# Kernel tuning notes

Measured on AMD Instinct MI355X. Metric: run time of the kernel, lower is better.

The kernel has to match this reference:

```python
import jax, jax.numpy as jnp
import numpy as np

TEMPERATURE = 0.5

def setup_inputs() -> dict:
    key = jax.random.key(0)
    ks = jax.random.split(key, 8)
    B, D, H, T, C = 4096, 1024, 4096, 8, 1000
    return {
        "x": jax.random.normal(ks[0], (B, D), jnp.float32),
        "signatures": jax.random.normal(ks[1], (T, D), jnp.float32) * 0.1,
        "W_up": jax.random.normal(ks[2], (T, H, D), jnp.float32) * (1.0 / np.sqrt(D)),
        "b_up": jax.random.normal(ks[3], (T, H), jnp.float32) * 0.01,
        "W_down": jax.random.normal(ks[4], (T, D, H), jnp.float32) * (1.0 / np.sqrt(H)),
        "b_down": jax.random.normal(ks[5], (T, D), jnp.float32) * 0.01,
        "W_cls": jax.random.normal(ks[6], (C, D), jnp.float32) * (1.0 / np.sqrt(D)),
        "b_cls": jax.random.normal(ks[7], (C,), jnp.float32) * 0.01,
    }

def reference(x, signatures, W_up, b_up, W_down, b_down, W_cls, b_cls):
    # Soft routing: scores (B, T), softmax weights at temperature 0.5
    scores = x @ signatures.T
    indices = jnp.argmax(scores, axis=-1)
    weights = jax.nn.softmax(scores / TEMPERATURE, axis=-1)
    # Batched per-tile FFN: Linear -> GELU(exact) -> Linear, all tiles at once
    h = jax.nn.gelu(jnp.einsum('bd,thd->bth', x, W_up) + b_up[None], approximate=False)  # (B,T,H)
    tile_out = jnp.einsum('bth,tdh->btd', h, W_down) + b_down[None]                      # (B,T,D)
    # Weighted combine + residual
    outputs = jnp.einsum('bt,btd->bd', weights, tile_out) + x
    logits = outputs @ W_cls.T + b_cls
    return logits, indices, weights
```

## Files before the change

### kernel.cpp

```cpp
#include <hip/hip_runtime.h>
#include <stdint.h>


typedef __attribute__((ext_vector_type(8))) __bf16 bf16x8;
typedef __attribute__((ext_vector_type(4))) float f32x4;

__device__ __forceinline__ unsigned short f2bf(float f) {
  union { float f; unsigned int u; } c; c.f = f;
  unsigned int u = c.u;
  u += 0x7FFFu + ((u >> 16) & 1u);
  return (unsigned short)(u >> 16);
}

__device__ __forceinline__ float gelu_fast(float x) {
  float x2 = x * x;
  float p = __builtin_fmaf(0.044715f * x2, x, x);
  float e = __expf(-1.5957691216057308f * p);
  return x / (1.0f + e);
}

__device__ __forceinline__ void gload16(const void* g, void* l) {
  __builtin_amdgcn_global_load_lds((const __attribute__((address_space(1))) void*)g,
                                   (__attribute__((address_space(3))) void*)l,
                                   16, 0, 0);
}

__global__ void conv_bf16(const float* __restrict__ in, unsigned short* __restrict__ out, int n4) {
  int i = blockIdx.x * blockDim.x + threadIdx.x;
  if (i >= n4) return;
  float4 v = reinterpret_cast<const float4*>(in)[i];
  ushort4 o;
  o.x = f2bf(v.x); o.y = f2bf(v.y); o.z = f2bf(v.z); o.w = f2bf(v.w);
  reinterpret_cast<ushort4*>(out)[i] = o;
}

__global__ void conv_wdn(const float* __restrict__ in, unsigned short* __restrict__ out) {
  int i = blockIdx.x * blockDim.x + threadIdx.x;
  int idx = i * 4;
  int h = idx & 4095;
  int d = (idx >> 12) & 1023;
  int t = idx >> 22;
  float4 v = *reinterpret_cast<const float4*>(in + (size_t)(t * 1024 + d) * 4096 + h);
  ushort4 o;
  o.x = f2bf(v.x); o.y = f2bf(v.y); o.z = f2bf(v.z); o.w = f2bf(v.w);
  *reinterpret_cast<ushort4*>(out + (size_t)d * 32768 + t * 4096 + h) = o;
}

__global__ void conv_wcls(const float* __restrict__ in, unsigned short* __restrict__ out) {
  int i = blockIdx.x * blockDim.x + threadIdx.x;
  int idx = i * 4;
  int row = idx >> 10;
  float4 v = make_float4(0.f, 0.f, 0.f, 0.f);
  if (row < 1000) v = *reinterpret_cast<const float4*>(in + row * 1024 + (idx & 1023));
  ushort4 o;
  o.x = f2bf(v.x); o.y = f2bf(v.y); o.z = f2bf(v.z); o.w = f2bf(v.w);
  reinterpret_cast<ushort4*>(out)[i] = o;
}

__global__ void score_init(const float* __restrict__ x, const float* __restrict__ sig,
                           const float* __restrict__ b_down,
                           float* __restrict__ w_ws, float* __restrict__ out_init,
                           float* __restrict__ w_out, float* __restrict__ idx_out) {
  const int b = blockIdx.x;
  const int tid = threadIdx.x;
  const int lane = tid & 63;
  const int wave = tid >> 6;
  const float* xr = x + (size_t)b * 1024;

  float p[8];
  #pragma unroll
  for (int t = 0; t < 8; ++t) p[t] = 0.f;

  for (int k = tid; k < 1024; k += 256) {
    float xv = xr[k];
    #pragma unroll
    for (int t = 0; t < 8; ++t) p[t] += xv * sig[t * 1024 + k];
  }
  #pragma unroll
  for (int t = 0; t < 8; ++t) {
    #pragma unroll
    for (int off = 32; off > 0; off >>= 1) p[t] += __shfl_down(p[t], off);
  }
  __shared__ float red[4][8];
  __shared__ float wsh[8];
  if (lane == 0) {
    #pragma unroll
    for (int t = 0; t < 8; ++t) red[wave][t] = p[t];
  }
  __syncthreads();
  if (tid == 0) {
    float s[8];
    #pragma unroll
    for (int t = 0; t < 8; ++t) s[t] = red[0][t] + red[1][t] + red[2][t] + red[3][t];
    int amax = 0; float mx = s[0];
    #pragma unroll
    for (int t = 1; t < 8; ++t) { if (s[t] > mx) { mx = s[t]; amax = t; } }
    float e[8], sum = 0.f;
    #pragma unroll
    for (int t = 0; t < 8; ++t) { e[t] = expf((s[t] - mx) * 2.0f); sum += e[t]; }
    float inv = 1.0f / sum;
    #pragma unroll
    for (int t = 0; t < 8; ++t) {
      float wv = e[t] * inv;
      wsh[t] = wv;
      w_out[(size_t)b * 8 + t] = wv;
      w_ws[(size_t)b * 8 + t] = wv;
    }
    idx_out[b] = (float)amax;
  }
  __syncthreads();
  for (int d = tid; d < 1024; d += 256) {
    float acc = xr[d];
    #pragma unroll
    for (int t = 0; t < 8; ++t) acc += wsh[t] * b_down[t * 1024 + d];
    out_init[(size_t)b * 1024 + d] = acc;
  }
}

template <int BN, int EPI>
__global__ __launch_bounds__(256, 2) void gemm_k(
    const unsigned short* __restrict__ A, int lda,
    const unsigned short* __restrict__ Bm, int ldb,
    int K,
    float* __restrict__ Cf, int ldc, int nvalid,
    unsigned short* __restrict__ Ch, int ldh,
    const float* __restrict__ bias,
    const float* __restrict__ wcol) {
  constexpr int FN = BN / 32;
  constexpr int AISS = 4;
  constexpr int BISS = BN / 32;

  __shared__ unsigned short As[128 * 64];
  __shared__ unsigned short Bs[BN * 64];

  if (EPI == 3) {
    size_t kz = (size_t)blockIdx.z * K;
    A += kz;
    Bm += kz;
    Cf += (size_t)blockIdx.z * 4194304;
  }

  const int tid  = threadIdx.x;
  const int lane = tid & 63;
  const int wave = tid >> 6;
  const int m0 = blockIdx.y * 128;
  const int n0 = blockIdx.x * BN;
  const int lr = lane & 15;
  const int lg = lane >> 4;
  const int wm = (wave >> 1) * 64;
  const int wn = (wave & 1) * (BN / 2);
  const int sw = (lr & 7) << 4;

  f32x4 acc[4][FN];
  #pragma unroll
  for (int i = 0; i < 4; ++i)
    #pragma unroll
    for (int j = 0; j < FN; ++j)
      #pragma unroll
      for (int q = 0; q < 4; ++q) acc[i][j][q] = 0.f;

  const char* Ab = (const char*)As;
  const char* Bb = (const char*)Bs;
  const int Lw = wave * 1024 + lane * 16;

  for (int k0 = 0; k0 < K; k0 += 64) {
    #pragma unroll
    for (int it = 0; it < AISS; ++it) {
      int L = it * 4096 + Lw;
      int row = L >> 7;
      int cb = (L & 127) ^ ((row & 7) << 4);
      const unsigned short* g = A + (size_t)(m0 + row) * lda + k0 + (cb >> 1);
      gload16(g, (void*)((char*)As + it * 4096 + wave * 1024));
    }
    #pragma unroll
    for (int it = 0; it < BISS; ++it) {
      int L = it * 4096 + Lw;
      int row = L >> 7;
      int cb = (L & 127) ^ ((row & 7) << 4);
      const unsigned short* g = Bm + (size_t)(n0 + row) * ldb + k0 + (cb >> 1);
      gload16(g, (void*)((char*)Bs + it * 4096 + wave * 1024));
    }
    asm volatile("s_waitcnt vmcnt(0)" ::: "memory");
    __syncthreads();

    #pragma unroll
    for (int kk = 0; kk < 2; ++kk) {
      bf16x8 a[4], bfr[FN];
      const int cbase = (kk << 6) + (lg << 4);
      #pragma unroll
      for (int mi = 0; mi < 4; ++mi) {
        int r = wm + mi * 16 + lr;
        a[mi] = *(const bf16x8*)(Ab + (r << 7) + (cbase ^ sw));
      }
      #pragma unroll
      for (int ni = 0; ni < FN; ++ni) {
        int r = wn + ni * 16 + lr;
        bfr[ni] = *(const bf16x8*)(Bb + (r << 7) + (cbase ^ sw));
      }
      #pragma unroll
      for (int mi = 0; mi < 4; ++mi)
        #pragma unroll
        for (int ni = 0; ni < FN; ++ni)
          acc[mi][ni] = __builtin_amdgcn_mfma_f32_16x16x32_bf16(a[mi], bfr[ni], acc[mi][ni], 0, 0, 0);
    }
    __syncthreads();
  }

  const int tblk = n0 >> 12;
  #pragma unroll
  for (int mi = 0; mi < 4; ++mi) {
    float wrow[4];
    if (EPI == 0) {
      #pragma unroll
      for (int r = 0; r < 4; ++r)
        wrow[r] = wcol[(size_t)(m0 + wm + mi * 16 + lg * 4 + r) * 8 + tblk];
    }
    #pragma unroll
    for (int ni = 0; ni < FN; ++ni) {
      int gn = n0 + wn + ni * 16 + lr;
      #pragma unroll
      for (int r = 0; r < 4; ++r) {
        int gm = m0 + wm + mi * 16 + lg * 4 + r;
        float v = acc[mi][ni][r];
        if (EPI == 0) {
          v += bias[gn];
          v = gelu_fast(v);
          v *= wrow[r];
          Ch[(size_t)gm * ldh + gn] = f2bf(v);
        } else if (EPI == 3) {
          Cf[(size_t)gm * ldc + gn] = v;
        } else {
          if (gn < nvalid) Cf[(size_t)gm * ldc + gn] = v + bias[gn];
        }
      }
    }
  }
}

__global__ void combine_k(const float* __restrict__ init, const float* __restrict__ parts,
                          unsigned short* __restrict__ out) {
  int i = blockIdx.x * blockDim.x + threadIdx.x;
  float4 s = reinterpret_cast<const float4*>(init)[i];
  #pragma unroll
  for (int z = 0; z < 4; ++z) {
    float4 p = reinterpret_cast<const float4*>(parts + (size_t)z * 4194304)[i];
    s.x += p.x; s.y += p.y; s.z += p.z; s.w += p.w;
  }
  ushort4 o;
  o.x = f2bf(s.x); o.y = f2bf(s.y); o.z = f2bf(s.z); o.w = f2bf(s.w);
  reinterpret_cast<ushort4*>(out)[i] = o;
}

extern "C" void kernel_launch(void* const* d_in, const int* in_sizes, int n_in,
                              void* d_out, int out_size, void* d_ws, size_t ws_size,
                              hipStream_t stream) {
  const float* x      = (const float*)d_in[0];
  const float* sig    = (const float*)d_in[1];
  const float* W_up   = (const float*)d_in[2];
  const float* b_up   = (const float*)d_in[3];
  const float* W_down = (const float*)d_in[4];
  const float* b_down = (const float*)d_in[5];
  const float* W_cls  = (const float*)d_in[6];
  const float* b_cls  = (const float*)d_in[7];

  float* outp    = (float*)d_out;
  float* logits  = outp;
  float* idx_out = outp + 4096000;
  float* w_out   = outp + 4096000 + 4096;

  char* ws = (char*)d_ws;
  unsigned short* xb    = (unsigned short*)ws;  ws += 8388608;
  unsigned short* hsc   = (unsigned short*)ws;  ws += 268435456;
  unsigned short* wupb  = (unsigned short*)ws;  ws += 67108864;
  unsigned short* wdnb  = (unsigned short*)ws;  ws += 67108864;
  unsigned short* wclsb = (unsigned short*)ws;  ws += 2097152;
  unsigned short* outb  = (unsigned short*)ws;  ws += 8388608;
  float* out_init       = (float*)ws;           ws += 16777216;
  float* parts          = (float*)ws;           ws += 67108864;
  float* w_ws           = (float*)ws;           ws += 131072;

  dim3 blk(256);

  conv_bf16<<<dim3(4096), blk, 0, stream>>>(x, xb, 1048576);
  score_init<<<dim3(4096), blk, 0, stream>>>(x, sig, b_down, w_ws, out_init, w_out, idx_out);
  conv_bf16<<<dim3(32768), blk, 0, stream>>>(W_up, wupb, 8388608);
  conv_wdn<<<dim3(32768), blk, 0, stream>>>(W_down, wdnb);
  conv_wcls<<<dim3(1024), blk, 0, stream>>>(W_cls, wclsb);

  gemm_k<128, 0><<<dim3(256, 32), blk, 0, stream>>>(
      xb, 1024, wupb, 1024, 1024,
      (float*)nullptr, 0, 0, hsc, 32768, b_up, w_ws);

  gemm_k<128, 3><<<dim3(8, 32, 4), blk, 0, stream>>>(
      hsc, 32768, wdnb, 32768, 8192,
      parts, 1024, 0, (unsigned short*)nullptr, 0, (const float*)nullptr, (const float*)nullptr);

  combine_k<<<dim3(4096), blk, 0, stream>>>(out_init, parts, outb);

  gemm_k<64, 2><<<dim3(16, 32), blk, 0, stream>>>(
      outb, 1024, wclsb, 1024, 1024,
      logits, 1000, 1000, (unsigned short*)nullptr, 0, b_cls, (const float*)nullptr);
}
```

Baseline: 834.7 us.

## Replace big GEMMs with 256x256-tile, 4-stage pipelined 8-wave kernel

The two large FFN GEMMs move to a new kernel with 512 threads, 256x256 output tiles, a 4-deep ring of LDS buffers loaded with K-steps of 32, and partial vmcnt waits, so global loads overlap MFMA work instead of stalling on every K-step. It also remaps block indices for L2 locality (grouping by f&7) and raises MFMA priority with setprio. The classifier GEMM keeps the old single-buffered kernel. The kernel uses 128KB of LDS per block, which limits occupancy, and the K-split GEMM now runs only 256 blocks, which may underfill the device.

```diff
diff --git a/kernel.cpp b/kernel.cpp
--- a/kernel.cpp
+++ b/kernel.cpp
@@ -70,7 +70,6 @@
   float p[8];
   #pragma unroll
   for (int t = 0; t < 8; ++t) p[t] = 0.f;
-
   for (int k = tid; k < 1024; k += 256) {
     float xv = xr[k];
     #pragma unroll
@@ -117,30 +116,155 @@
   }
 }
 
-template <int BN, int EPI>
-__global__ __launch_bounds__(256, 2) void gemm_k(
+template <int MODE>
+__global__ __launch_bounds__(512, 2) void gemm8(
     const unsigned short* __restrict__ A, int lda,
     const unsigned short* __restrict__ Bm, int ldb,
-    int K,
-    float* __restrict__ Cf, int ldc, int nvalid,
-    unsigned short* __restrict__ Ch, int ldh,
+    float* __restrict__ Cf,
+    unsigned short* __restrict__ Ch,
     const float* __restrict__ bias,
     const float* __restrict__ wcol) {
+  constexpr int NU = (MODE == 0) ? 32 : 256;
+  __shared__ char lds[131072];
+
+  const int tid = threadIdx.x;
+  const int f = blockIdx.x;
+  int m0, n0;
+  size_t koff = 0;
+  if (MODE == 0) {
+    int sf = (f & 7) * 256 + (f >> 3);
+    n0 = (sf >> 4) * 256;
+    m0 = (sf & 15) * 256;
+  } else {
+    int sf = (f & 7) * 32 + (f >> 3);
+    int z = sf >> 6, rem = sf & 63;
+    m0 = (rem >> 2) * 256;
+    n0 = (rem & 3) * 256;
+    koff = (size_t)z * 8192;
+    Cf += (size_t)z * 4194304;
+  }
+
+  const int srow = tid >> 2;
+  const int selem = ((tid & 3) * 8) ^ (((tid >> 3) & 3) * 8);
+  const unsigned short* Ag = A + (size_t)(m0 + srow) * lda + koff + selem;
+  const unsigned short* Bg = Bm + (size_t)(n0 + srow) * ldb + koff + selem;
+  const size_t ldaB = (size_t)128 * lda, ldbB = (size_t)128 * ldb;
+  char* ldsA = lds + tid * 16;
+  char* ldsB = lds + 65536 + tid * 16;
+
+  const int lane = tid & 63;
+  const int wave = tid >> 6;
+  const int lr = lane & 15, lg = lane >> 4;
+  const int wm = (wave >> 2) * 128;
+  const int wn = (wave & 3) * 64;
+
+  int offA[8], offB[4];
+  #pragma unroll
+  for (int mi = 0; mi < 8; ++mi) {
+    int r = wm + mi * 16 + lr;
+    offA[mi] = r * 64 + ((lg << 4) ^ (((r >> 1) & 3) << 4));
+  }
+  #pragma unroll
+  for (int ni = 0; ni < 4; ++ni) {
+    int r = wn + ni * 16 + lr;
+    offB[ni] = 65536 + r * 64 + ((lg << 4) ^ (((r >> 1) & 3) << 4));
+  }
+
+  f32x4 acc[8][4];
+  #pragma unroll
+  for (int i = 0; i < 8; ++i)
+    #pragma unroll
+    for (int j = 0; j < 4; ++j)
+      #pragma unroll
+      for (int q = 0; q < 4; ++q) acc[i][j][q] = 0.f;
+
+#define STAGE(v)                                                        \
+  {                                                                     \
+    const int s_ = ((v) & 3) * 16384;                                   \
+    const unsigned short* ga_ = Ag + (size_t)(v) * 32;                  \
+    const unsigned short* gb_ = Bg + (size_t)(v) * 32;                  \
+    gload16(ga_, ldsA + s_);                                            \
+    gload16(ga_ + ldaB, ldsA + s_ + 8192);                              \
+    gload16(gb_, ldsB + s_);                                            \
+    gload16(gb_ + ldbB, ldsB + s_ + 8192);                              \
+  }
+
+#define COMPUTE(u)                                                      \
+  {                                                                     \
+    const int s_ = ((u) & 3) * 16384;                                   \
+    bf16x8 av[8], bv[4];                                                \
+    _Pragma("unroll")                                                   \
+    for (int mi = 0; mi < 8; ++mi)                                      \
+      av[mi] = *(const bf16x8*)(lds + s_ + offA[mi]);                   \
+    _Pragma("unroll")                                                   \
+    for (int ni = 0; ni < 4; ++ni)                                      \
+      bv[ni] = *(const bf16x8*)(lds + s_ + offB[ni]);                   \
+    __builtin_amdgcn_s_setprio(1);                                      \
+    _Pragma("unroll")                                                   \
+    for (int mi = 0; mi < 8; ++mi)                                      \
+      _Pragma("unroll")                                                 \
+      for (int ni = 0; ni < 4; ++ni)                                    \
+        acc[mi][ni] = __builtin_amdgcn_mfma_f32_16x16x32_bf16(          \
+            av[mi], bv[ni], acc[mi][ni], 0, 0, 0);                      \
+    __builtin_amdgcn_s_setprio(0);                                      \
+  }
+
+  STAGE(0) STAGE(1) STAGE(2)
+
+  for (int u = 0; u < NU - 2; ++u) {
+    asm volatile("s_waitcnt vmcnt(8)" ::: "memory");
+    __builtin_amdgcn_s_barrier();
+    if (u + 3 < NU) STAGE(u + 3)
+    COMPUTE(u)
+  }
+  asm volatile("s_waitcnt vmcnt(4)" ::: "memory");
+  __builtin_amdgcn_s_barrier();
+  COMPUTE(NU - 2)
+  asm volatile("s_waitcnt vmcnt(0)" ::: "memory");
+  __builtin_amdgcn_s_barrier();
+  COMPUTE(NU - 1)
+
+#undef STAGE
+#undef COMPUTE
+
+  #pragma unroll
+  for (int mi = 0; mi < 8; ++mi) {
+    float wr[4];
+    if (MODE == 0) {
+      #pragma unroll
+      for (int r = 0; r < 4; ++r)
+        wr[r] = wcol[(size_t)(m0 + wm + mi * 16 + lg * 4 + r) * 8 + (n0 >> 12)];
+    }
+    #pragma unroll
+    for (int ni = 0; ni < 4; ++ni) {
+      int gn = n0 + wn + ni * 16 + lr;
+      #pragma unroll
+      for (int r = 0; r < 4; ++r) {
+        int gm = m0 + wm + mi * 16 + lg * 4 + r;
+        float v = acc[mi][ni][r];
+        if (MODE == 0) {
+          v += bias[gn];
+          v = gelu_fast(v) * wr[r];
+          Ch[(size_t)gm * 32768 + gn] = f2bf(v);
+        } else {
+          Cf[(size_t)gm * 1024 + gn] = v;
+        }
+      }
+    }
+  }
+}
+
+template <int BN>
+__global__ __launch_bounds__(256, 2) void gemm_cls(
+    const unsigned short* __restrict__ A, int lda,
+    const unsigned short* __restrict__ Bm, int ldb,
+    int K, float* __restrict__ Cf, int ldc, int nvalid,
+    const float* __restrict__ bias) {
   constexpr int FN = BN / 32;
-  constexpr int AISS = 4;
-  constexpr int BISS = BN / 32;
-
   __shared__ unsigned short As[128 * 64];
   __shared__ unsigned short Bs[BN * 64];
 
-  if (EPI == 3) {
-    size_t kz = (size_t)blockIdx.z * K;
-    A += kz;
-    Bm += kz;
-    Cf += (size_t)blockIdx.z * 4194304;
-  }
-
-  const int tid  = threadIdx.x;
+  const int tid = threadIdx.x;
   const int lane = tid & 63;
   const int wave = tid >> 6;
   const int m0 = blockIdx.y * 128;
@@ -165,20 +289,20 @@
 
   for (int k0 = 0; k0 < K; k0 += 64) {
     #pragma unroll
-    for (int it = 0; it < AISS; ++it) {
+    for (int it = 0; it < 4; ++it) {
       int L = it * 4096 + Lw;
       int row = L >> 7;
       int cb = (L & 127) ^ ((row & 7) << 4);
-      const unsigned short* g = A + (size_t)(m0 + row) * lda + k0 + (cb >> 1);
-      gload16(g, (void*)((char*)As + it * 4096 + wave * 1024));
-    }
-    #pragma unroll
-    for (int it = 0; it < BISS; ++it) {
+      gload16(A + (size_t)(m0 + row) * lda + k0 + (cb >> 1),
+              (void*)((char*)As + it * 4096 + wave * 1024));
+    }
+    #pragma unroll
+    for (int it = 0; it < FN; ++it) {
       int L = it * 4096 + Lw;
       int row = L >> 7;
       int cb = (L & 127) ^ ((row & 7) << 4);
-      const unsigned short* g = Bm + (size_t)(n0 + row) * ldb + k0 + (cb >> 1);
-      gload16(g, (void*)((char*)Bs + it * 4096 + wave * 1024));
+      gload16(Bm + (size_t)(n0 + row) * ldb + k0 + (cb >> 1),
+              (void*)((char*)Bs + it * 4096 + wave * 1024));
     }
     asm volatile("s_waitcnt vmcnt(0)" ::: "memory");
     __syncthreads();
@@ -188,15 +312,11 @@
       bf16x8 a[4], bfr[FN];
       const int cbase = (kk << 6) + (lg << 4);
       #pragma unroll
-      for (int mi = 0; mi < 4; ++mi) {
-        int r = wm + mi * 16 + lr;
-        a[mi] = *(const bf16x8*)(Ab + (r << 7) + (cbase ^ sw));
-      }
-      #pragma unroll
-      for (int ni = 0; ni < FN; ++ni) {
-        int r = wn + ni * 16 + lr;
-        bfr[ni] = *(const bf16x8*)(Bb + (r << 7) + (cbase ^ sw));
-      }
+      for (int mi = 0; mi < 4; ++mi)
+        a[mi] = *(const bf16x8*)(Ab + ((wm + mi * 16 + lr) << 7) + (cbase ^ sw));
+      #pragma unroll
+      for (int ni = 0; ni < FN; ++ni)
+        bfr[ni] = *(const bf16x8*)(Bb + ((wn + ni * 16 + lr) << 7) + (cbase ^ sw));
       #pragma unroll
       for (int mi = 0; mi < 4; ++mi)
         #pragma unroll
@@ -206,35 +326,17 @@
     __syncthreads();
   }
 
-  const int tblk = n0 >> 12;
-  #pragma unroll
-  for (int mi = 0; mi < 4; ++mi) {
-    float wrow[4];
-    if (EPI == 0) {
-      #pragma unroll
-      for (int r = 0; r < 4; ++r)
-        wrow[r] = wcol[(size_t)(m0 + wm + mi * 16 + lg * 4 + r) * 8 + tblk];
-    }
+  #pragma unroll
+  for (int mi = 0; mi < 4; ++mi)
     #pragma unroll
     for (int ni = 0; ni < FN; ++ni) {
       int gn = n0 + wn + ni * 16 + lr;
       #pragma unroll
       for (int r = 0; r < 4; ++r) {
         int gm = m0 + wm + mi * 16 + lg * 4 + r;
-        float v = acc[mi][ni][r];
-        if (EPI == 0) {
-          v += bias[gn];
-          v = gelu_fast(v);
-          v *= wrow[r];
-          Ch[(size_t)gm * ldh + gn] = f2bf(v);
-        } else if (EPI == 3) {
-          Cf[(size_t)gm * ldc + gn] = v;
-        } else {
-          if (gn < nvalid) Cf[(size_t)gm * ldc + gn] = v + bias[gn];
-        }
+        if (gn < nvalid) Cf[(size_t)gm * ldc + gn] = acc[mi][ni][r] + bias[gn];
       }
     }
-  }
 }
 
 __global__ void combine_k(const float* __restrict__ init, const float* __restrict__ parts,
@@ -287,17 +389,15 @@
   conv_wdn<<<dim3(32768), blk, 0, stream>>>(W_down, wdnb);
   conv_wcls<<<dim3(1024), blk, 0, stream>>>(W_cls, wclsb);
 
-  gemm_k<128, 0><<<dim3(256, 32), blk, 0, stream>>>(
-      xb, 1024, wupb, 1024, 1024,
-      (float*)nullptr, 0, 0, hsc, 32768, b_up, w_ws);
-
-  gemm_k<128, 3><<<dim3(8, 32, 4), blk, 0, stream>>>(
-      hsc, 32768, wdnb, 32768, 8192,
-      parts, 1024, 0, (unsigned short*)nullptr, 0, (const float*)nullptr, (const float*)nullptr);
+  gemm8<0><<<dim3(2048), dim3(512), 0, stream>>>(
+      xb, 1024, wupb, 1024, (float*)nullptr, hsc, b_up, w_ws);
+
+  gemm8<1><<<dim3(256), dim3(512), 0, stream>>>(
+      hsc, 32768, wdnb, 32768, parts, (unsigned short*)nullptr,
+      (const float*)nullptr, (const float*)nullptr);
 
   combine_k<<<dim3(4096), blk, 0, stream>>>(out_init, parts, outb);
 
-  gemm_k<64, 2><<<dim3(16, 32), blk, 0, stream>>>(
-      outb, 1024, wclsb, 1024, 1024,
-      logits, 1000, 1000, (unsigned short*)nullptr, 0, b_cls, (const float*)nullptr);
-}
+  gemm_cls<64><<<dim3(16, 32), blk, 0, stream>>>(
+      outb, 1024, wclsb, 1024, 1024, logits, 1000, 1000, b_cls);
+}
```

After: 787.1 us. 1.06x faster.

## Double-buffer LDS tiles in GEMM to overlap global loads with MFMA

Applied to the files above, without the earlier changes.

The GEMM main loop now uses two LDS slots for the A and B tiles. It issues the async global-to-LDS loads for the next k-step before computing on the current slot, and waits only on the older loads using a partial vmcnt. This is meant to hide global memory latency behind MFMA work instead of fully draining loads every iteration. In exchange LDS use per block doubles, which may limit occupancy against the two-blocks-per-CU launch bound, and correctness depends on the hand-tuned vmcnt counts and raw s_barrier placement.

```diff
diff --git a/kernel.cpp b/kernel.cpp
--- a/kernel.cpp
+++ b/kernel.cpp
@@ -70,7 +70,6 @@
   float p[8];
   #pragma unroll
   for (int t = 0; t < 8; ++t) p[t] = 0.f;
-
   for (int k = tid; k < 1024; k += 256) {
     float xv = xr[k];
     #pragma unroll
@@ -127,11 +126,10 @@
     const float* __restrict__ bias,
     const float* __restrict__ wcol) {
   constexpr int FN = BN / 32;
-  constexpr int AISS = 4;
   constexpr int BISS = BN / 32;
-
-  __shared__ unsigned short As[128 * 64];
-  __shared__ unsigned short Bs[BN * 64];
+  constexpr int BSLOT = BN * 128;
+
+  __shared__ char lds[32768 + 2 * BSLOT];
 
   if (EPI == 3) {
     size_t kz = (size_t)blockIdx.z * K;
@@ -159,52 +157,85 @@
       #pragma unroll
       for (int q = 0; q < 4; ++q) acc[i][j][q] = 0.f;
 
-  const char* Ab = (const char*)As;
-  const char* Bb = (const char*)Bs;
   const int Lw = wave * 1024 + lane * 16;
 
-  for (int k0 = 0; k0 < K; k0 += 64) {
-    #pragma unroll
-    for (int it = 0; it < AISS; ++it) {
-      int L = it * 4096 + Lw;
-      int row = L >> 7;
-      int cb = (L & 127) ^ ((row & 7) << 4);
-      const unsigned short* g = A + (size_t)(m0 + row) * lda + k0 + (cb >> 1);
-      gload16(g, (void*)((char*)As + it * 4096 + wave * 1024));
-    }
-    #pragma unroll
-    for (int it = 0; it < BISS; ++it) {
-      int L = it * 4096 + Lw;
-      int row = L >> 7;
-      int cb = (L & 127) ^ ((row & 7) << 4);
-      const unsigned short* g = Bm + (size_t)(n0 + row) * ldb + k0 + (cb >> 1);
-      gload16(g, (void*)((char*)Bs + it * 4096 + wave * 1024));
-    }
-    asm volatile("s_waitcnt vmcnt(0)" ::: "memory");
-    __syncthreads();
-
-    #pragma unroll
-    for (int kk = 0; kk < 2; ++kk) {
-      bf16x8 a[4], bfr[FN];
-      const int cbase = (kk << 6) + (lg << 4);
-      #pragma unroll
-      for (int mi = 0; mi < 4; ++mi) {
-        int r = wm + mi * 16 + lr;
-        a[mi] = *(const bf16x8*)(Ab + (r << 7) + (cbase ^ sw));
-      }
-      #pragma unroll
-      for (int ni = 0; ni < FN; ++ni) {
-        int r = wn + ni * 16 + lr;
-        bfr[ni] = *(const bf16x8*)(Bb + (r << 7) + (cbase ^ sw));
-      }
-      #pragma unroll
-      for (int mi = 0; mi < 4; ++mi)
-        #pragma unroll
-        for (int ni = 0; ni < FN; ++ni)
-          acc[mi][ni] = __builtin_amdgcn_mfma_f32_16x16x32_bf16(a[mi], bfr[ni], acc[mi][ni], 0, 0, 0);
-    }
-    __syncthreads();
-  }
+#define STAGE(k0_, s_)                                                    \
+  {                                                                       \
+    _Pragma("unroll")                                                     \
+    for (int it = 0; it < 4; ++it) {                                      \
+      int L = it * 4096 + Lw;                                             \
+      int row = L >> 7;                                                   \
+      int cb = (L & 127) ^ ((row & 7) << 4);                              \
+      gload16(A + (size_t)(m0 + row) * lda + (k0_) + (cb >> 1),           \
+              lds + (s_) * 16384 + it * 4096 + wave * 1024);              \
+    }                                                                     \
+    _Pragma("unroll")                                                     \
+    for (int it = 0; it < BISS; ++it) {                                   \
+      int L = it * 4096 + Lw;                                             \
+      int row = L >> 7;                                                   \
+      int cb = (L & 127) ^ ((row & 7) << 4);                              \
+      gload16(Bm + (size_t)(n0 + row) * ldb + (k0_) + (cb >> 1),          \
+              lds + 32768 + (s_) * BSLOT + it * 4096 + wave * 1024);      \
+    }                                                                     \
+  }
+
+#define COMP(s_)                                                          \
+  {                                                                       \
+    const char* Ab_ = lds + (s_) * 16384;                                 \
+    const char* Bb_ = lds + 32768 + (s_) * BSLOT;                         \
+    _Pragma("unroll")                                                     \
+    for (int kk = 0; kk < 2; ++kk) {                                      \
+      bf16x8 a[4], bfr[FN];                                               \
+      const int cbase = (kk << 6) + (lg << 4);                            \
+      _Pragma("unroll")                                                   \
+      for (int mi = 0; mi < 4; ++mi) {                                    \
+        int r = wm + mi * 16 + lr;                                        \
+        a[mi] = *(const bf16x8*)(Ab_ + (r << 7) + (cbase ^ sw));          \
+      }                                                                   \
+      _Pragma("unroll")                                                   \
+      for (int ni = 0; ni < FN; ++ni) {                                   \
+        int r = wn + ni * 16 + lr;                                        \
+        bfr[ni] = *(const bf16x8*)(Bb_ + (r << 7) + (cbase ^ sw));        \
+      }                                                                   \
+      _Pragma("unroll")                                                   \
+      for (int mi = 0; mi < 4; ++mi)                                      \
+        _Pragma("unroll")                                                 \
+        for (int ni = 0; ni < FN; ++ni)                                   \
+          acc[mi][ni] = __builtin_amdgcn_mfma_f32_16x16x32_bf16(          \
+              a[mi], bfr[ni], acc[mi][ni], 0, 0, 0);                      \
+    }                                                                     \
+  }
+
+#define VMW                                                               \
+  if constexpr (BN == 128) {                                              \
+    asm volatile("s_waitcnt vmcnt(8)" ::: "memory");                      \
+  } else {                                                                \
+    asm volatile("s_waitcnt vmcnt(6)" ::: "memory");                      \
+  }
+#define VM0  asm volatile("s_waitcnt vmcnt(0)" ::: "memory");
+#define BARR asm volatile("s_barrier" ::: "memory");
+
+  STAGE(0, 0)
+  int s = 0;
+  int k0 = 0;
+  for (; k0 + 64 < K; k0 += 64) {
+    BARR
+    STAGE(k0 + 64, s ^ 1)
+    VMW
+    BARR
+    COMP(s)
+    s ^= 1;
+  }
+  BARR
+  VM0
+  BARR
+  COMP(s)
+
+#undef STAGE
+#undef COMP
+#undef VMW
+#undef VM0
+#undef BARR
 
   const int tblk = n0 >> 12;
   #pragma unroll
```

After: 845.4 us. About the same (+1.3%).
